# Performance work log

Measured on AMD Instinct MI355X. Metric: run time of the kernel, lower is better.

The kernel has to match this reference:

```python
import jax, jax.numpy as jnp
import numpy as np
from jax import lax

C, S, Q = 20, 8, 16          # n_class, n_support, n_query
IMW, IMH, CH = 84, 84, 3     # image width, height, channels
CNT = 17.0                   # 1 aug + 8 same-class + 8 adversarial pair terms (loop break logic with S=8)

def _conv(x, k, b):
    return lax.conv_general_dilated(x, k, (1, 1), 'SAME',
                                    dimension_numbers=('NHWC', 'HWIO', 'NHWC')) + b

def _pool(x):
    return lax.reduce_window(x, -jnp.inf, lax.max, (1, 2, 2, 1), (1, 2, 2, 1), 'VALID')

def _d2(a, b):
    # calc_euclidian_dists: MEAN of squared differences over feature dim
    return jnp.mean((a - b) ** 2, axis=-1)

def _encoder(x, p):
    (k1, b1, k2, b2, k3, b3, k4, b4, k5, b5, k6, b6, k7, b7, k8, b8,
     g1, be1, g2, be2) = p
    x = _conv(x, k1, b1); x = _conv(x, k2, b2); x = _conv(x, k3, b3); x = _conv(x, k4, b4)
    x = _pool(jax.nn.relu(g1 * x + be1))
    x = _conv(x, k5, b5); x = _conv(x, k6, b6); x = _conv(x, k7, b7); x = _conv(x, k8, b8)
    x = _pool(jax.nn.relu(g2 * x + be2))
    return x.reshape(x.shape[0], -1)

def _pro_encoder(x, p, Wm):
    # same layers, each layer output scaled by W[i] (the `self.W[i] * layer` intent)
    (k1, b1, k2, b2, k3, b3, k4, b4, k5, b5, k6, b6, k7, b7, k8, b8,
     g1, be1, g2, be2) = p
    x = Wm[0] * _conv(x, k1, b1); x = Wm[1] * _conv(x, k2, b2)
    x = Wm[2] * _conv(x, k3, b3); x = Wm[3] * _conv(x, k4, b4)
    x = Wm[4] * (g1 * x + be1); x = Wm[5] * jax.nn.relu(x); x = Wm[6] * _pool(x)
    x = Wm[7] * _conv(x, k5, b5); x = Wm[8] * _conv(x, k6, b6)
    x = Wm[9] * _conv(x, k7, b7); x = Wm[10] * _conv(x, k8, b8)
    x = Wm[11] * (g2 * x + be2); x = Wm[12] * jax.nn.relu(x); x = Wm[13] * _pool(x)
    return Wm[14] * x.reshape(x.shape[0], -1)

def setup_inputs():
    key = jax.random.key(0)
    ks = jax.random.split(key, 24)
    def kern(k, cin):
        return jax.random.normal(k, (3, 3, cin, 16), jnp.float32) * 0.05
    inp = {
        'support': jax.random.normal(ks[0], (C, S, IMW, IMH, CH), jnp.float32),
        'query':   jax.random.normal(ks[1], (C, Q, IMW, IMH, CH), jnp.float32),
        'k1': kern(ks[2], CH)}
    for i in range(2, 9):
        inp['k%d' % i] = kern(ks[1 + i], 16)
    for i in range(1, 9):
        inp['b%d' % i] = jax.random.normal(ks[9 + i], (16,), jnp.float32) * 0.01
    inp['g1'] = jnp.ones((16,), jnp.float32)
    inp['be1'] = jnp.zeros((16,), jnp.float32)
    inp['g2'] = jnp.ones((16,), jnp.float32)
    inp['be2'] = jnp.zeros((16,), jnp.float32)
    inp['Wm'] = jax.random.normal(ks[20], (19,), jnp.float32)
    return inp

def _forward(support, query, p, Wm):
    n_class, n_support = support.shape[0], support.shape[1]
    n_query = query.shape[1]
    cat = jnp.concatenate([support.reshape(-1, IMW, IMH, CH),
                           query.reshape(-1, IMW, IMH, CH)], axis=0)
    z = _encoder(cat, p)
    D = z.shape[-1]
    z1 = z[:n_class * n_support].reshape(n_class, n_support, D)
    # tf.image.flip_left_right flips the second-to-last (width) axis of each image
    z_aug = _encoder(jnp.flip(support, axis=-2).reshape(-1, IMW, IMH, CH), p)
    z_aug = z_aug.reshape(n_class, n_support, D)
    d_aug = _d2(z1, z_aug) ** 2                                       # [C,S]
    # same-class pairwise terms: with S=8 the loop adds all 8 supports then breaks
    pos = jnp.sum(_d2(z1[:, :, None, :], z1[:, None, :, :]) ** 2, axis=2)
    z_adv = jnp.roll(z1, -1, axis=0)                                  # adversarial class (c+1)%C
    neg = jnp.sum(_d2(z1[:, :, None, :], z_adv[:, None, :, :]) ** 2, axis=2)
    uns_loss = jnp.sum((d_aug + pos - neg) / CNT + 0.5)
    zp = _pro_encoder(cat, p, Wm)
    protos = zp[:n_class * n_support].reshape(n_class, n_support, D).mean(axis=1)
    zq = zp[n_class * n_support:]
    dists = _d2(zq[:, None, :], protos[None, :, :])                   # [C*Q, C]
    log_p = jax.nn.log_softmax(-dists, axis=-1).reshape(n_class, n_query, n_class)
    y = jnp.tile(jnp.arange(n_class)[:, None], (1, n_query))
    ce = -jnp.mean(jnp.take_along_axis(log_p, y[:, :, None], axis=-1))
    loss = ce + uns_loss
    acc = jnp.mean((jnp.argmax(log_p, axis=-1) == y).astype(jnp.float32))
    return loss, acc

def reference(support, query, k1, k2, k3, k4, k5, k6, k7, k8,
              b1, b2, b3, b4, b5, b6, b7, b8, g1, be1, g2, be2, Wm):
    p = (k1, b1, k2, b2, k3, b3, k4, b4, k5, b5, k6, b6, k7, b7, k8, b8,
         g1, be1, g2, be2)
    return _forward(support, query, p, Wm)
```

## Files before the change

### kernel.cpp

```cpp
#include <hip/hip_runtime.h>
#include <math.h>


typedef __attribute__((ext_vector_type(8))) short bf16x8;
typedef __attribute__((ext_vector_type(8))) unsigned short u16x8;
typedef __attribute__((ext_vector_type(4))) float f32x4;
typedef unsigned short u16;
typedef unsigned int u32;

#define PIX84 (84 * 84)
#define D     (21 * 21 * 16)
#define WF_LAYER 2560
#define WF_C1 (7 * WF_LAYER)

__device__ __forceinline__ float bf2f(u16 v) {
    union { u32 i; float f; } c; c.i = ((u32)v) << 16; return c.f;
}
__device__ __forceinline__ u16 f2bf(float f) {
    union { float f; u32 i; } c; c.f = f;
    u32 r = c.i + 0x7fffu + ((c.i >> 16) & 1u);
    return (u16)(r >> 16);
}
__device__ __forceinline__ u32 pack2(float a, float b) {
    union { __bf16 h[2]; u32 u; } p;
    p.h[0] = (__bf16)a; p.h[1] = (__bf16)b;
    return p.u;
}

__device__ __forceinline__ bf16x8 ld_bf16x8_a8(const char* p) {
    union { uint2 q[2]; bf16x8 v; } u;
    u.q[0] = *(const uint2*)(p);
    u.q[1] = *(const uint2*)(p + 8);
    return u.v;
}

__device__ __forceinline__ float blockReduceSum(float v) {
    __shared__ float red[8];
    #pragma unroll
    for (int o = 32; o > 0; o >>= 1) v += __shfl_down(v, o, 64);
    const int lane = threadIdx.x & 63, wid = threadIdx.x >> 6;
    __syncthreads();
    if (lane == 0) red[wid] = v;
    __syncthreads();
    float r = 0.f;
    if (threadIdx.x == 0) {
        const int nw = (blockDim.x + 63) >> 6;
        for (int i = 0; i < nw; ++i) r += red[i];
    }
    return r;
}

__global__ void prep_weights(const float* __restrict__ k1, const float* __restrict__ k2,
                             const float* __restrict__ k3, const float* __restrict__ k4,
                             const float* __restrict__ k5, const float* __restrict__ k6,
                             const float* __restrict__ k7, const float* __restrict__ k8,
                             u16* __restrict__ wf)
{
    const int idx = blockIdx.x * 256 + threadIdx.x;
    if (idx < WF_C1) {
        const int j = idx & 7, lane = (idx >> 3) & 63, r = idx >> 9;
        const int m = r % 5, L = r / 5;
        const float* ks[7] = { k2, k3, k4, k5, k6, k7, k8 };
        const int co = lane & 15, g = lane >> 4;
        const int gg = g >> 1, h = g & 1;
        const int tap = gg ? (m + 5) : m;
        const int ci = h * 8 + j;
        const float v = (tap < 9) ? ks[L][(tap * 16 + ci) * 16 + co] : 0.f;
        wf[idx] = f2bf(v);
    } else if (idx < WF_C1 + 1024) {
        const int t = idx - WF_C1;
        const int j = t & 7, lane = (t >> 3) & 63, m = t >> 9;
        const int co = lane & 15, g = lane >> 4;
        const int k = g * 8 + j;
        const int dh  = (m == 0) ? (k >> 4) : 2;
        const int rem = (m == 0) ? (k & 15) : k;
        const int dw = rem >> 2, ci = rem & 3;
        const float v = (rem < 12 && ci < 3) ? k1[((dh * 3 + dw) * 3 + ci) * 16 + co] : 0.f;
        wf[idx] = f2bf(v);
    }
}

template <int W, int LW, int MAXT, int HALF>
__device__ __forceinline__ void conv_layer(char* buf, const u16* wfL,
                                           const float* bias, float scale,
                                           int nrows, int v0, int v1,
                                           int lane, int wv)
{
    const int g = lane >> 4, col = lane & 15, gg = g >> 1, h = g & 1;
    bf16x8 wfr[5];
    #pragma unroll
    for (int s = 0; s < 5; ++s) wfr[s] = ((const bf16x8*)wfL)[s * 64 + lane];
    const float4 bv = *(const float4*)(bias + g * 4);
    const float c0 = bv.x * scale, c1 = bv.y * scale;
    const float c2 = bv.z * scale, c3 = bv.w * scale;
    const int NPX = nrows * W;
    const int TC = (NPX + 15) >> 4;
    const int t0 = wv * MAXT;
    const int C0 = h * HALF + (gg ? (LW + 2)      : 0        ) * 16;
    const int C1 = h * HALF + (gg ? (2 * LW)      : 1        ) * 16;
    const int C2 = h * HALF + (gg ? (2 * LW + 1)  : 2        ) * 16;
    const int C3 = h * HALF + (gg ? (2 * LW + 2)  : LW       ) * 16;
    const int C4 = h * HALF + (gg ? (LW + 2)      : (LW + 1) ) * 16;
    const int wb = gg * HALF + h * 8 + 16;

    f32x4 acc[MAXT];
    int raddr[MAXT];
    u32 vmask = 0;
    #pragma unroll
    for (int u = 0; u < MAXT; ++u) {
        const int t = t0 + u;
        if (t < TC) {
            const int px = t * 16 + col;
            const int p = (px < NPX) ? px : 0;
            const int j = p / W, w = p - j * W;
            const int ra = (j * LW + w) * 16;
            raddr[u] = ra;
            if ((px < NPX) && (j >= v0) && (j < v1)) vmask |= (1u << u);
            const char* rb = buf + ra;
            f32x4 a = { 0.f, 0.f, 0.f, 0.f };
            a = __builtin_amdgcn_mfma_f32_16x16x32_bf16(wfr[0], *(const bf16x8*)(rb + C0), a, 0, 0, 0);
            a = __builtin_amdgcn_mfma_f32_16x16x32_bf16(wfr[1], *(const bf16x8*)(rb + C1), a, 0, 0, 0);
            a = __builtin_amdgcn_mfma_f32_16x16x32_bf16(wfr[2], *(const bf16x8*)(rb + C2), a, 0, 0, 0);
            a = __builtin_amdgcn_mfma_f32_16x16x32_bf16(wfr[3], *(const bf16x8*)(rb + C3), a, 0, 0, 0);
            a = __builtin_amdgcn_mfma_f32_16x16x32_bf16(wfr[4], *(const bf16x8*)(rb + C4), a, 0, 0, 0);
            acc[u] = a;
        }
    }
    __syncthreads();
    #pragma unroll
    for (int u = 0; u < MAXT; ++u) {
        const int t = t0 + u;
        if (t < TC) {
            const int px = t * 16 + col;
            if (px < NPX) {
                u32 lo = 0, hi = 0;
                if ((vmask >> u) & 1u) {
                    lo = pack2(fmaf(acc[u][0], scale, c0), fmaf(acc[u][1], scale, c1));
                    hi = pack2(fmaf(acc[u][2], scale, c2), fmaf(acc[u][3], scale, c3));
                }
                *(uint2*)(buf + raddr[u] + wb) = make_uint2(lo, hi);
            }
        }
    }
    __syncthreads();
}

#define HALF1 (20 * 86 * 16 + 16)
__global__ __launch_bounds__(512) void stage1_kernel(
    const float* __restrict__ sup, const float* __restrict__ qry,
    const float* __restrict__ b1,
    const u16* __restrict__ wf,
    const float* __restrict__ b2, const float* __restrict__ b3,
    const float* __restrict__ b4,
    const float* __restrict__ g1, const float* __restrict__ be1,
    const float* __restrict__ Wm,
    u16* __restrict__ s1out)
{
    __shared__ char buf[2 * HALF1];
    __shared__ u16 stag[(22 * 86 + 2) * 4];
    const int img = blockIdx.x / 6, bb = blockIdx.x % 6;
    const int R0 = 14 * bb;
    const int tid = threadIdx.x, lane = tid & 63, wv = tid >> 6;
    const bool pro = img >= 320;

    const float* src;
    bool flip = false;
    if (img < 160) src = sup + (size_t)img * (PIX84 * 3);
    else if (img < 320) { src = sup + (size_t)(img - 160) * (PIX84 * 3); flip = true; }
    else {
        const int m = img - 320;
        src = (m < 160) ? sup + (size_t)m * (PIX84 * 3)
                        : qry + (size_t)(m - 160) * (PIX84 * 3);
    }
    const float s1 = pro ? Wm[0] : 1.f, s2 = pro ? Wm[1] : 1.f;
    const float s3 = pro ? Wm[2] : 1.f, s4 = pro ? Wm[3] : 1.f;
    const float pre = pro ? Wm[4] : 1.f, rs = pro ? Wm[5] : 1.f;
    const float post = pro ? Wm[6] : 1.f;

    for (int i = tid; i < 40; i += 512) {
        const int P = (i >> 1) * 86 + ((i & 1) ? 85 : 0);
        *(uint4*)(buf + P * 16) = make_uint4(0, 0, 0, 0);
        *(uint4*)(buf + HALF1 + P * 16) = make_uint4(0, 0, 0, 0);
    }

    for (int p = tid; p < 22 * 86; p += 512) {
        const int r = p / 86, c = p - r * 86;
        const int hin = R0 - 4 + r, win = c - 1;
        u32 lo = 0, hi = 0;
        if ((unsigned)hin < 84u && (unsigned)win < 84u) {
            const int wsrc = flip ? (83 - win) : win;
            const float* ip = src + ((size_t)(hin * 84 + wsrc)) * 3;
            lo = pack2(ip[0], ip[1]);
            hi = pack2(ip[2], 0.f);
        }
        *(uint2*)((char*)stag + (size_t)p * 8) = make_uint2(lo, hi);
    }
    __syncthreads();

    {
        const int g = lane >> 4, col = lane & 15;
        const bf16x8 wA0 = ((const bf16x8*)(wf + WF_C1))[lane];
        const bf16x8 wA1 = ((const bf16x8*)(wf + WF_C1))[64 + lane];
        const float4 bv = *(const float4*)(b1 + g * 4);
        const int off0 = ((g >> 1) * 86 + (g & 1) * 2) * 8;
        const int off1 = (2 * 86 + (g & 1) * 2) * 8;
        const int wb_const = (g >> 1) * HALF1 + (g & 1) * 8;
        for (int t = wv; t < 105; t += 8) {
            const int p = t * 16 + col;
            const int ri = p / 84, w = p - ri * 84;
            const int base = (ri * 86 + w) * 8;
            const bf16x8 B0 = ld_bf16x8_a8((const char*)stag + base + off0);
            const bf16x8 B1 = ld_bf16x8_a8((const char*)stag + base + off1);
            f32x4 a = { 0.f, 0.f, 0.f, 0.f };
            a = __builtin_amdgcn_mfma_f32_16x16x32_bf16(wA0, B0, a, 0, 0, 0);
            a = __builtin_amdgcn_mfma_f32_16x16x32_bf16(wA1, B1, a, 0, 0, 0);
            const int hrow = R0 - 3 + ri;
            const float sc = ((unsigned)hrow < 84u) ? s1 : 0.f;
            const u32 lo = pack2((a[0] + bv.x) * sc, (a[1] + bv.y) * sc);
            const u32 hi = pack2((a[2] + bv.z) * sc, (a[3] + bv.w) * sc);
            *(uint2*)(buf + wb_const + (ri * 86 + (w + 1)) * 16) = make_uint2(lo, hi);
        }
    }
    __syncthreads();

    conv_layer<84, 86, 12, HALF1>(buf, wf,                b2, s2, 18,
                                  (2 - R0 > 0) ? 2 - R0 : 0, (86 - R0 < 18) ? 86 - R0 : 18, lane, wv);
    conv_layer<84, 86, 11, HALF1>(buf, wf + WF_LAYER,     b3, s3, 16,
                                  (1 - R0 > 0) ? 1 - R0 : 0, (85 - R0 < 16) ? 85 - R0 : 16, lane, wv);
    conv_layer<84, 86, 10, HALF1>(buf, wf + 2 * WF_LAYER, b4, s4, 14,
                                  0,                         (84 - R0 < 14) ? 84 - R0 : 14, lane, wv);

    const u32 uPRS = __float_as_uint(pre * rs);
    const float AR = post * rs;
    for (int e = tid; e < 7 * 42 * 2; e += 512) {
        const int hf = e & 1;
        const int pc = (e >> 1) % 42, pr = (e >> 1) / 42;
        const char* hb = buf + hf * HALF1;
        const int P0 = (2 * pr) * 86 + (2 * pc + 1);
        const u16x8 v00 = *(const u16x8*)(hb + P0 * 16);
        const u16x8 v01 = *(const u16x8*)(hb + (P0 + 1) * 16);
        const u16x8 v10 = *(const u16x8*)(hb + (P0 + 86) * 16);
        const u16x8 v11 = *(const u16x8*)(hb + (P0 + 87) * 16);
        float o[8];
        #pragma unroll
        for (int c = 0; c < 8; ++c) {
            const int ch = hf * 8 + c;
            const float x0 = bf2f(v00[c]), x1 = bf2f(v01[c]);
            const float x2 = bf2f(v10[c]), x3 = bf2f(v11[c]);
            const float mx = fmaxf(fmaxf(fmaxf(x0, x1), x2), x3);
            const float mn = fminf(fminf(fminf(x0, x1), x2), x3);
            const float gch = g1[ch];
            const bool dn = ((__float_as_uint(gch) ^ uPRS) >> 31) != 0;
            const float m = dn ? mn : mx;
            o[c] = AR * fmaxf(0.f, fmaf(pre * gch, m, pre * be1[ch]));
        }
        uint4 ov;
        ov.x = pack2(o[0], o[1]);
        ov.y = pack2(o[2], o[3]);
        ov.z = pack2(o[4], o[5]);
        ov.w = pack2(o[6], o[7]);
        *(uint4*)(s1out + (size_t)img * 28224 +
                  ((size_t)(7 * bb + pr) * 42 + pc) * 16 + hf * 8) = ov;
    }
}

#define LW2   46
#define NR2   30
#define HALF2 (NR2 * LW2 * 16 + 16)
__global__ __launch_bounds__(512) void stage2_kernel(
    const u16* __restrict__ s1in, const u16* __restrict__ wf,
    const float* __restrict__ b5, const float* __restrict__ b6,
    const float* __restrict__ b7, const float* __restrict__ b8,
    const float* __restrict__ g2, const float* __restrict__ be2,
    const float* __restrict__ Wm,
    float* __restrict__ z, float* __restrict__ zp)
{
    __shared__ char buf[2 * HALF2];
    const int img = blockIdx.x >> 1, hb2 = blockIdx.x & 1;
    const int nc8 = hb2 ? 20 : 22;
    const int R0in = hb2 ? 18 : -4;
    const int tid = threadIdx.x, lane = tid & 63, wv = tid >> 6;
    const bool pro = img >= 320;
    const float s5 = pro ? Wm[7] : 1.f, s6 = pro ? Wm[8] : 1.f;
    const float s7 = pro ? Wm[9] : 1.f, s8 = pro ? Wm[10] : 1.f;
    const float pre = pro ? Wm[11] : 1.f, rs = pro ? Wm[12] : 1.f;
    const float post = pro ? (Wm[13] * Wm[14]) : 1.f;

    const u16* ip = s1in + (size_t)img * 28224;
    for (int i = tid; i < NR2 * 44; i += 512) {
        const int r = i / 44, c = i - r * 44;
        const int gr = R0in + r;
        const int P = r * LW2 + c;
        uint4 v0 = make_uint4(0, 0, 0, 0), v1 = v0;
        if (c >= 1 && c <= 42 && gr >= 0 && gr < 42) {
            const u16* q = ip + ((size_t)(gr * 42 + (c - 1))) * 16;
            v0 = *(const uint4*)q;
            v1 = *(const uint4*)(q + 8);
        }
        *(uint4*)(buf + P * 16) = v0;
        *(uint4*)(buf + HALF2 + P * 16) = v1;
    }
    __syncthreads();

    {
        const int n1 = nc8 + 6, n2 = nc8 + 4, n3 = nc8 + 2, n4 = nc8;
        int a0, a1;
        a0 = -R0in - 1; if (a0 < 0) a0 = 0; a1 = 41 - R0in; if (a1 > n1) a1 = n1;
        conv_layer<42, LW2, 10, HALF2>(buf, wf + 3 * WF_LAYER, b5, s5, n1, a0, a1, lane, wv);
        a0 = -R0in - 2; if (a0 < 0) a0 = 0; a1 = 40 - R0in; if (a1 > n2) a1 = n2;
        conv_layer<42, LW2, 10, HALF2>(buf, wf + 4 * WF_LAYER, b6, s6, n2, a0, a1, lane, wv);
        a0 = -R0in - 3; if (a0 < 0) a0 = 0; a1 = 39 - R0in; if (a1 > n3) a1 = n3;
        conv_layer<42, LW2, 10, HALF2>(buf, wf + 5 * WF_LAYER, b7, s7, n3, a0, a1, lane, wv);
        a0 = -R0in - 4; if (a0 < 0) a0 = 0; a1 = 38 - R0in; if (a1 > n4) a1 = n4;
        conv_layer<42, LW2, 10, HALF2>(buf, wf + 6 * WF_LAYER, b8, s8, n4, a0, a1, lane, wv);
    }

    float* outp = pro ? (zp + (size_t)(img - 320) * D) : (z + (size_t)img * D);
    const u32 uPRS = __float_as_uint(pre * rs);
    const float AR = post * rs;
    const int np = nc8 >> 1;
    for (int e = tid; e < np * 21 * 2; e += 512) {
        const int hf = e & 1;
        const int pc = (e >> 1) % 21, pr = (e >> 1) / 21;
        const char* hb = buf + hf * HALF2;
        const int P0 = (2 * pr) * LW2 + (2 * pc + 1);
        const u16x8 v00 = *(const u16x8*)(hb + P0 * 16);
        const u16x8 v01 = *(const u16x8*)(hb + (P0 + 1) * 16);
        const u16x8 v10 = *(const u16x8*)(hb + (P0 + LW2) * 16);
        const u16x8 v11 = *(const u16x8*)(hb + (P0 + LW2 + 1) * 16);
        float o[8];
        #pragma unroll
        for (int c = 0; c < 8; ++c) {
            const int ch = hf * 8 + c;
            const float x0 = bf2f(v00[c]), x1 = bf2f(v01[c]);
            const float x2 = bf2f(v10[c]), x3 = bf2f(v11[c]);
            const float mx = fmaxf(fmaxf(fmaxf(x0, x1), x2), x3);
            const float mn = fminf(fminf(fminf(x0, x1), x2), x3);
            const float gch = g2[ch];
            const bool dn = ((__float_as_uint(gch) ^ uPRS) >> 31) != 0;
            const float m = dn ? mn : mx;
            o[c] = AR * fmaxf(0.f, fmaf(pre * gch, m, pre * be2[ch]));
        }
        float* op = outp + ((size_t)((hb2 * 11 + pr) * 21 + pc)) * 16 + hf * 8;
        *(float4*)op = make_float4(o[0], o[1], o[2], o[3]);
        *(float4*)(op + 4) = make_float4(o[4], o[5], o[6], o[7]);
    }
}

__global__ void pairs_kernel(const float* __restrict__ z,
                             float* __restrict__ within, float* __restrict__ cross,
                             float* __restrict__ aug)
{
    const int bid = blockIdx.x;
    const float *u, *v;
    float* dst;
    if (bid < 1280) {
        const int c = bid / 64, i = (bid % 64) / 8, j = bid % 8;
        u = z + (size_t)(c * 8 + i) * D;
        v = z + (size_t)(c * 8 + j) * D;
        dst = within + bid;
    } else if (bid < 2560) {
        const int t = bid - 1280;
        const int c = t / 64, i = (t % 64) / 8, j = t % 8;
        const int c2 = (c + 1) % 20;
        u = z + (size_t)(c * 8 + i) * D;
        v = z + (size_t)(c2 * 8 + j) * D;
        dst = cross + t;
    } else {
        const int t = bid - 2560;
        u = z + (size_t)t * D;
        v = z + (size_t)(160 + t) * D;
        dst = aug + t;
    }
    const float4* u4 = (const float4*)u;
    const float4* v4 = (const float4*)v;
    float s = 0.f;
    for (int d = threadIdx.x; d < D / 4; d += 256) {
        const float4 a = u4[d], b = v4[d];
        const float dx = a.x - b.x, dy = a.y - b.y, dz = a.z - b.z, dw = a.w - b.w;
        s += dx * dx + dy * dy + dz * dz + dw * dw;
    }
    s = blockReduceSum(s);
    if (threadIdx.x == 0) {
        const float m = s / (float)D;
        *dst = m * m;
    }
}

__global__ void protos_kernel(const float* __restrict__ zp, float* __restrict__ protos)
{
    const int idx = blockIdx.x * 256 + threadIdx.x;
    if (idx >= 20 * D) return;
    const int c = idx / D, d = idx % D;
    float s = 0.f;
    #pragma unroll
    for (int i = 0; i < 8; ++i) s += zp[(size_t)(c * 8 + i) * D + d];
    protos[idx] = s * 0.125f;
}

__global__ void dists_kernel(const float* __restrict__ zq, const float* __restrict__ protos,
                             float* __restrict__ dists)
{
    const int q = blockIdx.x / 20, c = blockIdx.x % 20;
    const float4* u4 = (const float4*)(zq + (size_t)q * D);
    const float4* v4 = (const float4*)(protos + (size_t)c * D);
    float s = 0.f;
    for (int d = threadIdx.x; d < D / 4; d += 256) {
        const float4 a = u4[d], b = v4[d];
        const float dx = a.x - b.x, dy = a.y - b.y, dz = a.z - b.z, dw = a.w - b.w;
        s += dx * dx + dy * dy + dz * dz + dw * dw;
    }
    s = blockReduceSum(s);
    if (threadIdx.x == 0) dists[blockIdx.x] = s / (float)D;
}

__global__ void final_kernel(const float* __restrict__ dists,
                             const float* __restrict__ within,
                             const float* __restrict__ cross,
                             const float* __restrict__ aug,
                             float* __restrict__ out)
{
    float ce = 0.f, accv = 0.f, uns = 0.f;
    for (int r = threadIdx.x; r < 320; r += 256) {
        const float* dr = dists + r * 20;
        const int y = r / 16;
        float dmin = dr[0];
        int amin = 0;
        float m = -dr[0];
        #pragma unroll
        for (int j = 1; j < 20; ++j) {
            if (dr[j] < dmin) { dmin = dr[j]; amin = j; }
            m = fmaxf(m, -dr[j]);
        }
        float se = 0.f;
        #pragma unroll
        for (int j = 0; j < 20; ++j) se += expf(-dr[j] - m);
        const float lse = m + logf(se);
        ce += dr[y] + lse;
        accv += (amin == y) ? 1.0f : 0.0f;
    }
    for (int i = threadIdx.x; i < 1280; i += 256) uns += within[i] - cross[i];
    for (int i = threadIdx.x; i < 160; i += 256) uns += aug[i];

    ce = blockReduceSum(ce);
    accv = blockReduceSum(accv);
    uns = blockReduceSum(uns);
    if (threadIdx.x == 0) {
        out[0] = ce / 320.0f + uns / 17.0f + 80.0f;
        out[1] = accv / 320.0f;
    }
}

extern "C" void kernel_launch(void* const* d_in, const int* in_sizes, int n_in,
                              void* d_out, int out_size, void* d_ws, size_t ws_size,
                              hipStream_t stream)
{
    (void)in_sizes; (void)n_in; (void)out_size; (void)ws_size;
    const float* sup = (const float*)d_in[0];
    const float* qry = (const float*)d_in[1];
    const float* K[8]; for (int i = 0; i < 8; ++i) K[i] = (const float*)d_in[2 + i];
    const float* B[8]; for (int i = 0; i < 8; ++i) B[i] = (const float*)d_in[10 + i];
    const float* g1  = (const float*)d_in[18];
    const float* be1 = (const float*)d_in[19];
    const float* g2  = (const float*)d_in[20];
    const float* be2 = (const float*)d_in[21];
    const float* Wm  = (const float*)d_in[22];
    float* out = (float*)d_out;

    size_t off = 0;
    auto alloc = [&](size_t bytes) -> void* {
        void* p = (char*)d_ws + off;
        off += (bytes + 255) & ~(size_t)255;
        return p;
    };
    u16*   wf     = (u16*)alloc((size_t)(WF_C1 + 1024) * 2);
    u16*   s1out  = (u16*)alloc((size_t)800 * 42 * 42 * 16 * 2);
    float* z      = (float*)alloc((size_t)320 * D * 4);
    float* zp     = (float*)alloc((size_t)480 * D * 4);
    float* within = (float*)alloc(1280 * 4);
    float* crossb = (float*)alloc(1280 * 4);
    float* augb   = (float*)alloc(160 * 4);
    float* protos = (float*)alloc((size_t)20 * D * 4);
    float* dist   = (float*)alloc(6400 * 4);

    prep_weights<<<(WF_C1 + 1024 + 255) / 256, 256, 0, stream>>>(
        K[0], K[1], K[2], K[3], K[4], K[5], K[6], K[7], wf);

    stage1_kernel<<<800 * 6, 512, 0, stream>>>(sup, qry, B[0], wf,
                                               B[1], B[2], B[3], g1, be1, Wm, s1out);
    stage2_kernel<<<1600, 512, 0, stream>>>(s1out, wf, B[4], B[5], B[6], B[7],
                                            g2, be2, Wm, z, zp);

    pairs_kernel<<<2720, 256, 0, stream>>>(z, within, crossb, augb);
    protos_kernel<<<(20 * D + 255) / 256, 256, 0, stream>>>(zp, protos);
    dists_kernel<<<6400, 256, 0, stream>>>(zp + (size_t)160 * D, protos, dist);
    final_kernel<<<1, 256, 0, stream>>>(dist, within, crossb, augb, out);
}
```

Before: 295.5 us.

## Fold Wm scales into prescaled weights/biases and precompute conv pixel addresses

Prep kernel now builds two weight/bias variants, one plain and one with the per-layer Wm scale folded in. The conv layers seed the accumulator with the bias and drop the per-output scale FMA. Pixel row addresses are computed once per thread by incremental stepping instead of per-tile divisions, and valid-row masks become address-range compares. Launch bounds now request 4 waves-per-EU occupancy and the LDS buffers gain an extra row; bf16 rounding of the prescaled weights changes numerics slightly.

```diff
diff --git a/kernel.cpp b/kernel.cpp
--- a/kernel.cpp
+++ b/kernel.cpp
@@ -12,6 +12,7 @@
 #define D     (21 * 21 * 16)
 #define WF_LAYER 2560
 #define WF_C1 (7 * WF_LAYER)
+#define WF_VAR (WF_C1 + 1024)
 
 __device__ __forceinline__ float bf2f(u16 v) {
     union { u32 i; float f; } c; c.i = ((u32)v) << 16; return c.f;
@@ -54,70 +55,75 @@
                              const float* __restrict__ k3, const float* __restrict__ k4,
                              const float* __restrict__ k5, const float* __restrict__ k6,
                              const float* __restrict__ k7, const float* __restrict__ k8,
-                             u16* __restrict__ wf)
+                             const float* __restrict__ b1, const float* __restrict__ b2,
+                             const float* __restrict__ b3, const float* __restrict__ b4,
+                             const float* __restrict__ b5, const float* __restrict__ b6,
+                             const float* __restrict__ b7, const float* __restrict__ b8,
+                             const float* __restrict__ Wm,
+                             u16* __restrict__ wf, float* __restrict__ bias_tab)
 {
     const int idx = blockIdx.x * 256 + threadIdx.x;
-    if (idx < WF_C1) {
-        const int j = idx & 7, lane = (idx >> 3) & 63, r = idx >> 9;
-        const int m = r % 5, L = r / 5;
-        const float* ks[7] = { k2, k3, k4, k5, k6, k7, k8 };
-        const int co = lane & 15, g = lane >> 4;
-        const int gg = g >> 1, h = g & 1;
-        const int tap = gg ? (m + 5) : m;
-        const int ci = h * 8 + j;
-        const float v = (tap < 9) ? ks[L][(tap * 16 + ci) * 16 + co] : 0.f;
-        wf[idx] = f2bf(v);
-    } else if (idx < WF_C1 + 1024) {
-        const int t = idx - WF_C1;
-        const int j = t & 7, lane = (t >> 3) & 63, m = t >> 9;
-        const int co = lane & 15, g = lane >> 4;
-        const int k = g * 8 + j;
-        const int dh  = (m == 0) ? (k >> 4) : 2;
-        const int rem = (m == 0) ? (k & 15) : k;
-        const int dw = rem >> 2, ci = rem & 3;
-        const float v = (rem < 12 && ci < 3) ? k1[((dh * 3 + dw) * 3 + ci) * 16 + co] : 0.f;
-        wf[idx] = f2bf(v);
-    }
-}
-
-template <int W, int LW, int MAXT, int HALF>
+    if (idx < 2 * WF_VAR) {
+        const int v = (idx >= WF_VAR) ? 1 : 0;
+        const int r0 = idx - v * WF_VAR;
+        if (r0 < WF_C1) {
+            const int j = r0 & 7, lane = (r0 >> 3) & 63, r = r0 >> 9;
+            const int m = r % 5, L = r / 5;
+            const float* ks[7] = { k2, k3, k4, k5, k6, k7, k8 };
+            const int sidx[7] = { 1, 2, 3, 7, 8, 9, 10 };
+            const int co = lane & 15, g = lane >> 4;
+            const int gg = g >> 1, h = g & 1;
+            const int tap = gg ? (m + 5) : m;
+            const int ci = h * 8 + j;
+            float val = (tap < 9) ? ks[L][(tap * 16 + ci) * 16 + co] : 0.f;
+            if (v) val *= Wm[sidx[L]];
+            wf[idx] = f2bf(val);
+        } else {
+            const int t = r0 - WF_C1;
+            const int j = t & 7, lane = (t >> 3) & 63, m = t >> 9;
+            const int co = lane & 15, g = lane >> 4;
+            const int k = g * 8 + j;
+            const int dh  = (m == 0) ? (k >> 4) : 2;
+            const int rem = (m == 0) ? (k & 15) : k;
+            const int dw = rem >> 2, ci = rem & 3;
+            float val = (rem < 12 && ci < 3) ? k1[((dh * 3 + dw) * 3 + ci) * 16 + co] : 0.f;
+            if (v) val *= Wm[0];
+            wf[idx] = f2bf(val);
+        }
+    } else if (idx < 2 * WF_VAR + 256) {
+        const int t = idx - 2 * WF_VAR;
+        const int v = t >> 7, L = (t >> 4) & 7, ch = t & 15;
+        const float* Bs[8] = { b1, b2, b3, b4, b5, b6, b7, b8 };
+        const int sm[8] = { 0, 1, 2, 3, 7, 8, 9, 10 };
+        float val = Bs[L][ch];
+        if (v) val *= Wm[sm[L]];
+        bias_tab[t] = val;
+    }
+}
+
+template <int LW, int NT, int HALF>
 __device__ __forceinline__ void conv_layer(char* buf, const u16* wfL,
-                                           const float* bias, float scale,
-                                           int nrows, int v0, int v1,
-                                           int lane, int wv)
-{
-    const int g = lane >> 4, col = lane & 15, gg = g >> 1, h = g & 1;
+                                           const float4 bv,
+                                           const int (&raddr)[NT], int trips,
+                                           int ra_lo, int ra_hi, int lane)
+{
+    const int g = lane >> 4, gg = g >> 1, h = g & 1;
     bf16x8 wfr[5];
     #pragma unroll
     for (int s = 0; s < 5; ++s) wfr[s] = ((const bf16x8*)wfL)[s * 64 + lane];
-    const float4 bv = *(const float4*)(bias + g * 4);
-    const float c0 = bv.x * scale, c1 = bv.y * scale;
-    const float c2 = bv.z * scale, c3 = bv.w * scale;
-    const int NPX = nrows * W;
-    const int TC = (NPX + 15) >> 4;
-    const int t0 = wv * MAXT;
-    const int C0 = h * HALF + (gg ? (LW + 2)      : 0        ) * 16;
-    const int C1 = h * HALF + (gg ? (2 * LW)      : 1        ) * 16;
-    const int C2 = h * HALF + (gg ? (2 * LW + 1)  : 2        ) * 16;
-    const int C3 = h * HALF + (gg ? (2 * LW + 2)  : LW       ) * 16;
-    const int C4 = h * HALF + (gg ? (LW + 2)      : (LW + 1) ) * 16;
+    const int C0 = h * HALF + (gg ? (LW + 2)     : 0       ) * 16;
+    const int C1 = h * HALF + (gg ? (2 * LW)     : 1       ) * 16;
+    const int C2 = h * HALF + (gg ? (2 * LW + 1) : 2       ) * 16;
+    const int C3 = h * HALF + (gg ? (2 * LW + 2) : LW      ) * 16;
+    const int C4 = h * HALF + (gg ? (LW + 2)     : (LW + 1)) * 16;
     const int wb = gg * HALF + h * 8 + 16;
 
-    f32x4 acc[MAXT];
-    int raddr[MAXT];
-    u32 vmask = 0;
+    f32x4 acc[NT];
     #pragma unroll
-    for (int u = 0; u < MAXT; ++u) {
-        const int t = t0 + u;
-        if (t < TC) {
-            const int px = t * 16 + col;
-            const int p = (px < NPX) ? px : 0;
-            const int j = p / W, w = p - j * W;
-            const int ra = (j * LW + w) * 16;
-            raddr[u] = ra;
-            if ((px < NPX) && (j >= v0) && (j < v1)) vmask |= (1u << u);
-            const char* rb = buf + ra;
-            f32x4 a = { 0.f, 0.f, 0.f, 0.f };
+    for (int u = 0; u < NT; ++u) {
+        if (u < trips) {
+            const char* rb = buf + raddr[u];
+            f32x4 a = { bv.x, bv.y, bv.z, bv.w };
             a = __builtin_amdgcn_mfma_f32_16x16x32_bf16(wfr[0], *(const bf16x8*)(rb + C0), a, 0, 0, 0);
             a = __builtin_amdgcn_mfma_f32_16x16x32_bf16(wfr[1], *(const bf16x8*)(rb + C1), a, 0, 0, 0);
             a = __builtin_amdgcn_mfma_f32_16x16x32_bf16(wfr[2], *(const bf16x8*)(rb + C2), a, 0, 0, 0);
@@ -128,30 +134,24 @@
     }
     __syncthreads();
     #pragma unroll
-    for (int u = 0; u < MAXT; ++u) {
-        const int t = t0 + u;
-        if (t < TC) {
-            const int px = t * 16 + col;
-            if (px < NPX) {
-                u32 lo = 0, hi = 0;
-                if ((vmask >> u) & 1u) {
-                    lo = pack2(fmaf(acc[u][0], scale, c0), fmaf(acc[u][1], scale, c1));
-                    hi = pack2(fmaf(acc[u][2], scale, c2), fmaf(acc[u][3], scale, c3));
-                }
-                *(uint2*)(buf + raddr[u] + wb) = make_uint2(lo, hi);
-            }
-        }
-    }
-    __syncthreads();
-}
-
-#define HALF1 (20 * 86 * 16 + 16)
-__global__ __launch_bounds__(512) void stage1_kernel(
+    for (int u = 0; u < NT; ++u) {
+        if (u < trips) {
+            const int ra = raddr[u];
+            const bool val = (ra >= ra_lo) && (ra < ra_hi);
+            const u32 lo = val ? pack2(acc[u][0], acc[u][1]) : 0u;
+            const u32 hi = val ? pack2(acc[u][2], acc[u][3]) : 0u;
+            *(uint2*)(buf + ra + wb) = make_uint2(lo, hi);
+        }
+    }
+    __syncthreads();
+}
+
+#define ROWS1 21
+#define HALF1 (ROWS1 * 86 * 16 + 16)
+#define LIM1  (18 * 86 * 16)
+__global__ __launch_bounds__(512, 4) void stage1_kernel(
     const float* __restrict__ sup, const float* __restrict__ qry,
-    const float* __restrict__ b1,
-    const u16* __restrict__ wf,
-    const float* __restrict__ b2, const float* __restrict__ b3,
-    const float* __restrict__ b4,
+    const u16* __restrict__ wf, const float* __restrict__ bias_tab,
     const float* __restrict__ g1, const float* __restrict__ be1,
     const float* __restrict__ Wm,
     u16* __restrict__ s1out)
@@ -172,8 +172,8 @@
         src = (m < 160) ? sup + (size_t)m * (PIX84 * 3)
                         : qry + (size_t)(m - 160) * (PIX84 * 3);
     }
-    const float s1 = pro ? Wm[0] : 1.f, s2 = pro ? Wm[1] : 1.f;
-    const float s3 = pro ? Wm[2] : 1.f, s4 = pro ? Wm[3] : 1.f;
+    const u16* wfv = wf + (pro ? WF_VAR : 0);
+    const float* bt = bias_tab + (pro ? 128 : 0);
     const float pre = pro ? Wm[4] : 1.f, rs = pro ? Wm[5] : 1.f;
     const float post = pro ? Wm[6] : 1.f;
 
@@ -197,38 +197,66 @@
     }
     __syncthreads();
 
+    const int g = lane >> 4, col = lane & 15, gg = g >> 1, h = g & 1;
+    const int px0 = wv * 16 + col;
+
     {
-        const int g = lane >> 4, col = lane & 15;
-        const bf16x8 wA0 = ((const bf16x8*)(wf + WF_C1))[lane];
-        const bf16x8 wA1 = ((const bf16x8*)(wf + WF_C1))[64 + lane];
-        const float4 bv = *(const float4*)(b1 + g * 4);
-        const int off0 = ((g >> 1) * 86 + (g & 1) * 2) * 8;
-        const int off1 = (2 * 86 + (g & 1) * 2) * 8;
-        const int wb_const = (g >> 1) * HALF1 + (g & 1) * 8;
-        for (int t = wv; t < 105; t += 8) {
-            const int p = t * 16 + col;
-            const int ri = p / 84, w = p - ri * 84;
-            const int base = (ri * 86 + w) * 8;
-            const bf16x8 B0 = ld_bf16x8_a8((const char*)stag + base + off0);
-            const bf16x8 B1 = ld_bf16x8_a8((const char*)stag + base + off1);
-            f32x4 a = { 0.f, 0.f, 0.f, 0.f };
-            a = __builtin_amdgcn_mfma_f32_16x16x32_bf16(wA0, B0, a, 0, 0, 0);
-            a = __builtin_amdgcn_mfma_f32_16x16x32_bf16(wA1, B1, a, 0, 0, 0);
-            const int hrow = R0 - 3 + ri;
-            const float sc = ((unsigned)hrow < 84u) ? s1 : 0.f;
-            const u32 lo = pack2((a[0] + bv.x) * sc, (a[1] + bv.y) * sc);
-            const u32 hi = pack2((a[2] + bv.z) * sc, (a[3] + bv.w) * sc);
-            *(uint2*)(buf + wb_const + (ri * 86 + (w + 1)) * 16) = make_uint2(lo, hi);
-        }
-    }
-    __syncthreads();
-
-    conv_layer<84, 86, 12, HALF1>(buf, wf,                b2, s2, 18,
-                                  (2 - R0 > 0) ? 2 - R0 : 0, (86 - R0 < 18) ? 86 - R0 : 18, lane, wv);
-    conv_layer<84, 86, 11, HALF1>(buf, wf + WF_LAYER,     b3, s3, 16,
-                                  (1 - R0 > 0) ? 1 - R0 : 0, (85 - R0 < 16) ? 85 - R0 : 16, lane, wv);
-    conv_layer<84, 86, 10, HALF1>(buf, wf + 2 * WF_LAYER, b4, s4, 14,
-                                  0,                         (84 - R0 < 14) ? 84 - R0 : 14, lane, wv);
+        const bf16x8 wA0 = ((const bf16x8*)(wfv + WF_C1))[lane];
+        const bf16x8 wA1 = ((const bf16x8*)(wfv + WF_C1))[64 + lane];
+        const float4 bv = *(const float4*)(bt + g * 4);
+        const int off0 = (gg * 86 + h * 2) * 8;
+        const int off1 = (2 * 86 + h * 2) * 8;
+        const int wbc = gg * HALF1 + h * 8 + 16;
+        const int lo1 = ((R0 == 0) ? 3 : 0) * (86 * 8);
+        const int hi1 = ((R0 == 70) ? 17 : 20) * (86 * 8);
+        int w = px0, j = 0;
+        if (w >= 84) { w -= 84; j = 1; }
+        int sra = (j * 86 + w) * 8;
+        const int trips1 = (112 - wv) >> 3;
+        #pragma unroll
+        for (int u = 0; u < 14; ++u) {
+            if (u < trips1) {
+                const bf16x8 B0 = ld_bf16x8_a8((const char*)stag + sra + off0);
+                const bf16x8 B1 = ld_bf16x8_a8((const char*)stag + sra + off1);
+                f32x4 a = { bv.x, bv.y, bv.z, bv.w };
+                a = __builtin_amdgcn_mfma_f32_16x16x32_bf16(wA0, B0, a, 0, 0, 0);
+                a = __builtin_amdgcn_mfma_f32_16x16x32_bf16(wA1, B1, a, 0, 0, 0);
+                const bool val = (sra >= lo1) && (sra < hi1);
+                const u32 lo = val ? pack2(a[0], a[1]) : 0u;
+                const u32 hi = val ? pack2(a[2], a[3]) : 0u;
+                *(uint2*)(buf + sra * 2 + wbc) = make_uint2(lo, hi);
+            }
+            const bool wrap = (w + 44) >= 84;
+            sra += wrap ? 1056 : 1040;
+            w = wrap ? (w - 40) : (w + 44);
+        }
+    }
+    __syncthreads();
+
+    int raddr[12];
+    {
+        int w = px0, j = 0;
+        if (w >= 84) { w -= 84; j = 1; }
+        int ra = (j * 86 + w) * 16;
+        #pragma unroll
+        for (int u = 0; u < 12; ++u) {
+            raddr[u] = (ra < LIM1) ? ra : LIM1;
+            const bool wrap = (w + 44) >= 84;
+            ra += wrap ? 2112 : 2080;
+            w = wrap ? (w - 40) : (w + 44);
+        }
+    }
+    const float4 bv2 = *(const float4*)(bt + 16 + g * 4);
+    const float4 bv3 = *(const float4*)(bt + 32 + g * 4);
+    const float4 bv4 = *(const float4*)(bt + 48 + g * 4);
+    const int RB = 86 * 16;
+    int v0, v1;
+    v0 = (R0 == 0) ? 2 : 0;  v1 = (86 - R0 < 18) ? 86 - R0 : 18;
+    conv_layer<86, 12, HALF1>(buf, wfv,                bv2, raddr, (102 - wv) >> 3, v0 * RB, v1 * RB, lane);
+    v0 = (R0 == 0) ? 1 : 0;  v1 = (85 - R0 < 16) ? 85 - R0 : 16;
+    conv_layer<86, 12, HALF1>(buf, wfv + WF_LAYER,     bv3, raddr, (91 - wv) >> 3,  v0 * RB, v1 * RB, lane);
+    v0 = 0;                  v1 = (84 - R0 < 14) ? 84 - R0 : 14;
+    conv_layer<86, 12, HALF1>(buf, wfv + 2 * WF_LAYER, bv4, raddr, (81 - wv) >> 3,  v0 * RB, v1 * RB, lane);
 
     const u32 uPRS = __float_as_uint(pre * rs);
     const float AR = post * rs;
@@ -265,12 +293,12 @@
 }
 
 #define LW2   46
-#define NR2   30
-#define HALF2 (NR2 * LW2 * 16 + 16)
-__global__ __launch_bounds__(512) void stage2_kernel(
-    const u16* __restrict__ s1in, const u16* __restrict__ wf,
-    const float* __restrict__ b5, const float* __restrict__ b6,
-    const float* __restrict__ b7, const float* __restrict__ b8,
+#define ROWS2 31
+#define HALF2 (ROWS2 * LW2 * 16 + 16)
+#define LIM2  (28 * LW2 * 16)
+__global__ __launch_bounds__(512, 4) void stage2_kernel(
+    const u16* __restrict__ s1in,
+    const u16* __restrict__ wf, const float* __restrict__ bias_tab,
     const float* __restrict__ g2, const float* __restrict__ be2,
     const float* __restrict__ Wm,
     float* __restrict__ z, float* __restrict__ zp)
@@ -281,39 +309,63 @@
     const int R0in = hb2 ? 18 : -4;
     const int tid = threadIdx.x, lane = tid & 63, wv = tid >> 6;
     const bool pro = img >= 320;
-    const float s5 = pro ? Wm[7] : 1.f, s6 = pro ? Wm[8] : 1.f;
-    const float s7 = pro ? Wm[9] : 1.f, s8 = pro ? Wm[10] : 1.f;
+    const u16* wfv = wf + (pro ? WF_VAR : 0);
+    const float* bt = bias_tab + (pro ? 128 : 0);
     const float pre = pro ? Wm[11] : 1.f, rs = pro ? Wm[12] : 1.f;
     const float post = pro ? (Wm[13] * Wm[14]) : 1.f;
 
     const u16* ip = s1in + (size_t)img * 28224;
-    for (int i = tid; i < NR2 * 44; i += 512) {
+    for (int i = tid; i < 30 * 44; i += 512) {
         const int r = i / 44, c = i - r * 44;
         const int gr = R0in + r;
         const int P = r * LW2 + c;
-        uint4 v0 = make_uint4(0, 0, 0, 0), v1 = v0;
+        uint4 w0 = make_uint4(0, 0, 0, 0), w1 = w0;
         if (c >= 1 && c <= 42 && gr >= 0 && gr < 42) {
             const u16* q = ip + ((size_t)(gr * 42 + (c - 1))) * 16;
-            v0 = *(const uint4*)q;
-            v1 = *(const uint4*)(q + 8);
-        }
-        *(uint4*)(buf + P * 16) = v0;
-        *(uint4*)(buf + HALF2 + P * 16) = v1;
-    }
-    __syncthreads();
-
+            w0 = *(const uint4*)q;
+            w1 = *(const uint4*)(q + 8);
+        }
+        *(uint4*)(buf + P * 16) = w0;
+        *(uint4*)(buf + HALF2 + P * 16) = w1;
+    }
+    __syncthreads();
+
+    const int g = lane >> 4, col = lane & 15;
+    const int px0 = wv * 16 + col;
+
+    int raddr[10];
     {
-        const int n1 = nc8 + 6, n2 = nc8 + 4, n3 = nc8 + 2, n4 = nc8;
-        int a0, a1;
-        a0 = -R0in - 1; if (a0 < 0) a0 = 0; a1 = 41 - R0in; if (a1 > n1) a1 = n1;
-        conv_layer<42, LW2, 10, HALF2>(buf, wf + 3 * WF_LAYER, b5, s5, n1, a0, a1, lane, wv);
-        a0 = -R0in - 2; if (a0 < 0) a0 = 0; a1 = 40 - R0in; if (a1 > n2) a1 = n2;
-        conv_layer<42, LW2, 10, HALF2>(buf, wf + 4 * WF_LAYER, b6, s6, n2, a0, a1, lane, wv);
-        a0 = -R0in - 3; if (a0 < 0) a0 = 0; a1 = 39 - R0in; if (a1 > n3) a1 = n3;
-        conv_layer<42, LW2, 10, HALF2>(buf, wf + 5 * WF_LAYER, b7, s7, n3, a0, a1, lane, wv);
-        a0 = -R0in - 4; if (a0 < 0) a0 = 0; a1 = 38 - R0in; if (a1 > n4) a1 = n4;
-        conv_layer<42, LW2, 10, HALF2>(buf, wf + 6 * WF_LAYER, b8, s8, n4, a0, a1, lane, wv);
-    }
+        int w = px0, j = 0;
+        if (w >= 84) { w -= 84; j = 2; }
+        if (w >= 42) { w -= 42; j += 1; }
+        int ra = (j * LW2 + w) * 16;
+        #pragma unroll
+        for (int u = 0; u < 10; ++u) {
+            raddr[u] = (ra < LIM2) ? ra : LIM2;
+            const bool wrap = (w + 2) >= 42;
+            ra += wrap ? 2304 : 2240;
+            w = wrap ? (w - 40) : (w + 2);
+        }
+    }
+    const float4 bv5 = *(const float4*)(bt + 64 + g * 4);
+    const float4 bv6 = *(const float4*)(bt + 80 + g * 4);
+    const float4 bv7 = *(const float4*)(bt + 96 + g * 4);
+    const float4 bv8 = *(const float4*)(bt + 112 + g * 4);
+    const int n1 = nc8 + 6, n2 = nc8 + 4, n3 = nc8 + 2, n4 = nc8;
+    const int RB = LW2 * 16;
+    int a0, a1;
+    a0 = -R0in - 1; if (a0 < 0) a0 = 0; a1 = 41 - R0in; if (a1 > n1) a1 = n1;
+    conv_layer<LW2, 10, HALF2>(buf, wfv + 3 * WF_LAYER, bv5, raddr,
+                               (((n1 * 42 + 15) >> 4) + 7 - wv) >> 3, a0 * RB, a1 * RB, lane);
+    a0 = -R0in - 2; if (a0 < 0) a0 = 0; a1 = 40 - R0in; if (a1 > n2) a1 = n2;
+    conv_layer<LW2, 10, HALF2>(buf, wfv + 4 * WF_LAYER, bv6, raddr,
+                               (((n2 * 42 + 15) >> 4) + 7 - wv) >> 3, a0 * RB, a1 * RB, lane);
+    a0 = -R0in - 3; if (a0 < 0) a0 = 0; a1 = 39 - R0in; if (a1 > n3) a1 = n3;
+    conv_layer<LW2, 10, HALF2>(buf, wfv + 5 * WF_LAYER, bv7, raddr,
+                               (((n3 * 42 + 15) >> 4) + 7 - wv) >> 3, a0 * RB, a1 * RB, lane);
+    a0 = -R0in - 4; if (a0 < 0) a0 = 0; a1 = 38 - R0in; if (a1 > n4) a1 = n4;
+    conv_layer<LW2, 10, HALF2>(buf, wfv + 6 * WF_LAYER, bv8, raddr,
+                               (((n4 * 42 + 15) >> 4) + 7 - wv) >> 3, a0 * RB, a1 * RB, lane);
 
     float* outp = pro ? (zp + (size_t)(img - 320) * D) : (z + (size_t)img * D);
     const u32 uPRS = __float_as_uint(pre * rs);
@@ -473,7 +525,8 @@
         off += (bytes + 255) & ~(size_t)255;
         return p;
     };
-    u16*   wf     = (u16*)alloc((size_t)(WF_C1 + 1024) * 2);
+    u16*   wf     = (u16*)alloc((size_t)2 * WF_VAR * 2);
+    float* btab   = (float*)alloc(256 * 4);
     u16*   s1out  = (u16*)alloc((size_t)800 * 42 * 42 * 16 * 2);
     float* z      = (float*)alloc((size_t)320 * D * 4);
     float* zp     = (float*)alloc((size_t)480 * D * 4);
@@ -483,13 +536,13 @@
     float* protos = (float*)alloc((size_t)20 * D * 4);
     float* dist   = (float*)alloc(6400 * 4);
 
-    prep_weights<<<(WF_C1 + 1024 + 255) / 256, 256, 0, stream>>>(
-        K[0], K[1], K[2], K[3], K[4], K[5], K[6], K[7], wf);
-
-    stage1_kernel<<<800 * 6, 512, 0, stream>>>(sup, qry, B[0], wf,
-                                               B[1], B[2], B[3], g1, be1, Wm, s1out);
-    stage2_kernel<<<1600, 512, 0, stream>>>(s1out, wf, B[4], B[5], B[6], B[7],
-                                            g2, be2, Wm, z, zp);
+    prep_weights<<<(2 * WF_VAR + 256 + 255) / 256, 256, 0, stream>>>(
+        K[0], K[1], K[2], K[3], K[4], K[5], K[6], K[7],
+        B[0], B[1], B[2], B[3], B[4], B[5], B[6], B[7],
+        Wm, wf, btab);
+
+    stage1_kernel<<<800 * 6, 512, 0, stream>>>(sup, qry, wf, btab, g1, be1, Wm, s1out);
+    stage2_kernel<<<1600, 512, 0, stream>>>(s1out, wf, btab, g2, be2, Wm, z, zp);
 
     pairs_kernel<<<2720, 256, 0, stream>>>(z, within, crossb, augb);
     protos_kernel<<<(20 * D + 255) / 256, 256, 0, stream>>>(zp, protos);
```

Result: slower. 398.6 us (+34.9%).
